# Optimization experiments

Hardware: AMD Instinct MI355X
Metric: run time of the kernel (lower is better)

Reference implementation:

```python
import jax, jax.numpy as jnp
import numpy as np

D_MODEL = 512
D_FF = 2048
VOCAB = 32000
B, N = 2, 384
EPS = 1e-6


def positional_encoding(n, d):
    pos = np.arange(n)[:, None].astype(np.float64)
    i = np.arange(d)[None, :]
    ang = pos / np.power(10000.0, (2 * (i // 2)) / np.float32(d))
    ang[:, 0::2] = np.sin(ang[:, 0::2])
    ang[:, 1::2] = np.cos(ang[:, 1::2])
    return jnp.asarray(ang, dtype=jnp.float32)  # [n, d]


def layer_norm(x, gamma, beta):
    mu = jnp.mean(x, axis=-1, keepdims=True)
    var = jnp.mean(jnp.square(x - mu), axis=-1, keepdims=True)
    return (x - mu) / jnp.sqrt(var + EPS) * gamma + beta


def setup_inputs() -> dict:
    key = jax.random.key(0)
    ks = jax.random.split(key, 12)
    s = 0.02
    return {
        "tokens": jax.random.randint(ks[0], (B, N), 0, VOCAB, dtype=jnp.int32),
        "emb": jax.random.normal(ks[1], (VOCAB, D_MODEL), jnp.float32) * s,
        "Wq": jax.random.normal(ks[2], (D_MODEL, D_MODEL), jnp.float32) * s,
        "bq": jnp.zeros((D_MODEL,), jnp.float32),
        "Wk": jax.random.normal(ks[3], (D_MODEL, D_MODEL), jnp.float32) * s,
        "bk": jnp.zeros((D_MODEL,), jnp.float32),
        "Wv": jax.random.normal(ks[4], (D_MODEL, D_MODEL), jnp.float32) * s,
        "bv": jnp.zeros((D_MODEL,), jnp.float32),
        "attn_scale": jax.random.normal(ks[5], (D_MODEL,), jnp.float32) * 0.05,
        "Wo": jax.random.normal(ks[6], (D_MODEL, D_MODEL), jnp.float32) * s,
        "bo": jnp.zeros((D_MODEL,), jnp.float32),
        "g1": jnp.ones((D_MODEL,), jnp.float32),
        "beta1": jnp.zeros((D_MODEL,), jnp.float32),
        "W1": jax.random.normal(ks[7], (D_MODEL, D_FF), jnp.float32) * s,
        "bf1": jnp.zeros((D_FF,), jnp.float32),
        "W2": jax.random.normal(ks[8], (D_FF, D_MODEL), jnp.float32) * s,
        "bf2": jnp.zeros((D_MODEL,), jnp.float32),
        "g2": jnp.ones((D_MODEL,), jnp.float32),
        "beta2": jnp.zeros((D_MODEL,), jnp.float32),
    }


def reference(tokens, emb, Wq, bq, Wk, bk, Wv, bv, attn_scale, Wo, bo,
              g1, beta1, W1, bf1, W2, bf2, g2, beta2):
    # Embedding + scaled positional encoding
    x = emb[tokens] * jnp.sqrt(jnp.float32(D_MODEL))  # [B, N, D]
    x = x + positional_encoding(N, D_MODEL)[None, :, :]

    # Additive (Bahdanau) self-attention
    q = x @ Wq + bq
    k = x @ Wk + bk  # note: original swaps key/value Dense layers; math-equivalent
    v = x @ Wv + bv
    # scores[b,i,j] = sum_d scale[d] * tanh(q[b,i,d] + k[b,j,d])  -> [B,N,N]
    scores = jnp.einsum("d,bijd->bij", attn_scale,
                        jnp.tanh(q[:, :, None, :] + k[:, None, :, :]))
    weights = jax.nn.softmax(scores, axis=-1)
    attn = jnp.einsum("bij,bjd->bid", weights, v)
    attn = attn @ Wo + bo
    x = layer_norm(x + attn, g1, beta1)

    # Feedforward + residual + LayerNorm
    h = jax.nn.relu(x @ W1 + bf1)
    y = h @ W2 + bf2
    return layer_norm(x + y, g2, beta2)
```

## Files before the change

### kernel.cpp

```cpp
#include <hip/hip_runtime.h>
#include <hip/hip_bf16.h>
#include <math.h>

#define D_MODEL 512
#define D_FF    2048
#define NBATCH  2
#define NSEQ    384
#define NROWS   (NBATCH * NSEQ)
#define LN_EPS  1e-6f

typedef __attribute__((ext_vector_type(8))) short short8;
typedef __attribute__((ext_vector_type(4))) short short4v;
typedef __attribute__((ext_vector_type(4))) float f32x4;
typedef __hip_bfloat16 bf16;

static __device__ __forceinline__ short bfb(float x) {
    bf16 h = __float2bfloat16(x);
    return *reinterpret_cast<short*>(&h);
}

__global__ __launch_bounds__(256) void wt_all_kernel(
    const float* __restrict__ Wq, const float* __restrict__ Wk,
    const float* __restrict__ Wv, const float* __restrict__ Wo,
    const float* __restrict__ W1, const float* __restrict__ W2,
    bf16* __restrict__ wqt, bf16* __restrict__ wkt, bf16* __restrict__ wvt,
    bf16* __restrict__ wot, bf16* __restrict__ w1t, bf16* __restrict__ w2t)
{
    int t = blockIdx.x;
    const float* W; bf16* Wt; int K, N, bx, by;
    if (t < 1024) {
        int w = t >> 8, rem = t & 255;
        W  = (w == 0) ? Wq  : (w == 1) ? Wk  : (w == 2) ? Wv  : Wo;
        Wt = (w == 0) ? wqt : (w == 1) ? wkt : (w == 2) ? wvt : wot;
        K = 512; N = 512; bx = rem & 15; by = rem >> 4;
    } else if (t < 2048) {
        int rem = t - 1024;
        W = W1; Wt = w1t; K = 512; N = 2048; bx = rem & 63; by = rem >> 6;
    } else {
        int rem = t - 2048;
        W = W2; Wt = w2t; K = 2048; N = 512; bx = rem & 15; by = rem >> 4;
    }

    __shared__ float tile[32][33];
    int tx = threadIdx.x & 31, ty = threadIdx.x >> 5;
    #pragma unroll
    for (int r = ty; r < 32; r += 8)
        tile[r][tx] = W[(size_t)(by * 32 + r) * N + bx * 32 + tx];
    __syncthreads();
    #pragma unroll
    for (int r = ty; r < 32; r += 8)
        Wt[(size_t)(bx * 32 + r) * K + by * 32 + tx] = __float2bfloat16(tile[tx][r]);
}

__global__ __launch_bounds__(256) void embed_pe_kernel(
    const int* __restrict__ tokens, const float* __restrict__ emb,
    float* __restrict__ x, bf16* __restrict__ xb)
{
    int row = blockIdx.x;
    int n   = row % NSEQ;
    int tok = tokens[row];
    const float sqrtD = 22.627416997969522f;
    for (int d = threadIdx.x; d < D_MODEL; d += 256) {
        float e = emb[tok * D_MODEL + d] * sqrtD;
        int   i2   = d & ~1;
        float expo = (float)i2 / (float)D_MODEL;
        float ang  = (float)n * powf(10000.0f, -expo);
        float pe   = (d & 1) ? cosf(ang) : sinf(ang);
        float val  = e + pe;
        x [(size_t)row * D_MODEL + d] = val;
        xb[(size_t)row * D_MODEL + d] = __float2bfloat16(val);
    }
}

__global__ __launch_bounds__(256) void qkv_mfma_kernel(
    const bf16* __restrict__ A,
    const bf16* __restrict__ wqt, const bf16* __restrict__ wkt, const bf16* __restrict__ wvt,
    const float* __restrict__ bq, const float* __restrict__ bk, const float* __restrict__ bv,
    float* __restrict__ aexp, float* __restrict__ bexp, bf16* __restrict__ vT)
{
    int z = blockIdx.z;
    const bf16*  Wt   = (z == 0) ? wqt : (z == 1) ? wkt : wvt;
    const float* bias = (z == 0) ? bq  : (z == 1) ? bk  : bv;

    int lane = threadIdx.x & 63, wid = threadIdx.x >> 6;
    int rowBase = blockIdx.y * 32 + (wid >> 1) * 16;
    int colBase = blockIdx.x * 64 + (wid & 1) * 32;

    const bf16* Ap  = A  + (size_t)(rowBase + (lane & 15)) * D_MODEL + ((lane >> 4) << 3);
    const bf16* Bp0 = Wt + (size_t)(colBase + (lane & 15)) * D_MODEL + ((lane >> 4) << 3);
    const bf16* Bp1 = Bp0 + (size_t)16 * D_MODEL;

    f32x4 acc0 = {0.f, 0.f, 0.f, 0.f};
    f32x4 acc1 = {0.f, 0.f, 0.f, 0.f};

    #pragma unroll 4
    for (int k0 = 0; k0 < D_MODEL; k0 += 32) {
        short8 a  = *reinterpret_cast<const short8*>(Ap  + k0);
        short8 b0 = *reinterpret_cast<const short8*>(Bp0 + k0);
        short8 b1 = *reinterpret_cast<const short8*>(Bp1 + k0);
        acc0 = __builtin_amdgcn_mfma_f32_16x16x32_bf16(a, b0, acc0, 0, 0, 0);
        acc1 = __builtin_amdgcn_mfma_f32_16x16x32_bf16(a, b1, acc1, 0, 0, 0);
    }

    int crow = rowBase + ((lane >> 4) << 2);
    int ccol = colBase + (lane & 15);

    if (z < 2) {
        float* C = (z == 0) ? aexp : bexp;
        #pragma unroll
        for (int r = 0; r < 4; ++r) {
            int row = crow + r;
            #pragma unroll
            for (int j = 0; j < 2; ++j) {
                int col = ccol + j * 16;
                float val = (j == 0 ? acc0[r] : acc1[r]) + bias[col];
                C[(size_t)row * D_MODEL + col] = __expf(2.0f * val);
            }
        }
    } else {
        int bb = crow / NSEQ;
        int jr = crow - bb * NSEQ;
        #pragma unroll
        for (int j = 0; j < 2; ++j) {
            int col = ccol + j * 16;
            short4v pk;
            #pragma unroll
            for (int r = 0; r < 4; ++r)
                pk[r] = bfb((j == 0 ? acc0[r] : acc1[r]) + bias[col]);
            size_t idx = ((size_t)bb * D_MODEL + col) * NSEQ + jr;
            *reinterpret_cast<short4v*>((short*)vT + idx) = pk;
        }
    }
}

__global__ __launch_bounds__(512) void score_kernel(
    const float* __restrict__ aexp, const float* __restrict__ bexp,
    const float* __restrict__ scale, bf16* __restrict__ E,
    float* __restrict__ Sp)
{
    int ip   = blockIdx.x;
    int half = blockIdx.y;
    int row0 = ip * 2;
    int b    = row0 / NSEQ;
    int tid  = threadIdx.x;
    int lane = tid & 63, wid = tid >> 6;

    __shared__ float sred[8][2];

    const float* a0p = aexp + (size_t)row0 * D_MODEL + lane * 8;
    float4 A0 = *(const float4*)(a0p);
    float4 A1 = *(const float4*)(a0p + 4);
    float4 B0 = *(const float4*)(a0p + D_MODEL);
    float4 B1 = *(const float4*)(a0p + D_MODEL + 4);
    const float* sp0 = scale + lane * 8;
    float4 S0 = *(const float4*)(sp0);
    float4 S1 = *(const float4*)(sp0 + 4);
    float a0[8] = {A0.x,A0.y,A0.z,A0.w,A1.x,A1.y,A1.z,A1.w};
    float a1[8] = {B0.x,B0.y,B0.z,B0.w,B1.x,B1.y,B1.z,B1.w};
    float sv[8] = {-2.0f*S0.x,-2.0f*S0.y,-2.0f*S0.z,-2.0f*S0.w,
                   -2.0f*S1.x,-2.0f*S1.y,-2.0f*S1.z,-2.0f*S1.w};

    const float* kb = bexp + (size_t)b * NSEQ * D_MODEL + lane * 8;
    int jb = half * 192 + wid;

    float es0 = 0.0f, es1 = 0.0f;

    for (int t = 0; t < 24; t += 2) {
        int j0 = jb + t * 8;
        int j1 = j0 + 8;
        const float4* kp0 = (const float4*)(kb + (size_t)j0 * D_MODEL);
        const float4* kp1 = (const float4*)(kb + (size_t)j1 * D_MODEL);
        float4 x0v = kp0[0], x1v = kp0[1];
        float4 y0v = kp1[0], y1v = kp1[1];
        float b0[8] = {x0v.x,x0v.y,x0v.z,x0v.w,x1v.x,x1v.y,x1v.z,x1v.w};
        float b1[8] = {y0v.x,y0v.y,y0v.z,y0v.w,y1v.x,y1v.y,y1v.z,y1v.w};

        float t00 = 0.f, t01 = 0.f, t10 = 0.f, t11 = 0.f;
        #pragma unroll
        for (int u = 0; u < 8; ++u) {
            float r0 = __builtin_amdgcn_rcpf(fmaf(a0[u], b0[u], 1.0f));
            float r1 = __builtin_amdgcn_rcpf(fmaf(a1[u], b0[u], 1.0f));
            float r2 = __builtin_amdgcn_rcpf(fmaf(a0[u], b1[u], 1.0f));
            float r3 = __builtin_amdgcn_rcpf(fmaf(a1[u], b1[u], 1.0f));
            t00 = fmaf(sv[u], r0, t00);
            t01 = fmaf(sv[u], r1, t01);
            t10 = fmaf(sv[u], r2, t10);
            t11 = fmaf(sv[u], r3, t11);
        }
        #pragma unroll
        for (int off = 1; off < 64; off <<= 1) {
            t00 += __shfl_xor(t00, off, 64);
            t01 += __shfl_xor(t01, off, 64);
            t10 += __shfl_xor(t10, off, 64);
            t11 += __shfl_xor(t11, off, 64);
        }
        float e00 = __expf(t00);
        float e01 = __expf(t01);
        float e10 = __expf(t10);
        float e11 = __expf(t11);
        if (lane == 0) {
            E[(size_t)row0 * NSEQ + j0]       = __float2bfloat16(e00);
            E[(size_t)(row0 + 1) * NSEQ + j0] = __float2bfloat16(e01);
            E[(size_t)row0 * NSEQ + j1]       = __float2bfloat16(e10);
            E[(size_t)(row0 + 1) * NSEQ + j1] = __float2bfloat16(e11);
        }
        es0 += e00 + e10;
        es1 += e01 + e11;
    }

    if (lane == 0) { sred[wid][0] = es0; sred[wid][1] = es1; }
    __syncthreads();
    if (tid < 2) {
        float s = 0.0f;
        #pragma unroll
        for (int w = 0; w < 8; ++w) s += sred[w][tid];
        Sp[(size_t)(row0 + tid) * 2 + half] = s;
    }
}

__global__ __launch_bounds__(256) void pv_mfma_kernel(
    const bf16* __restrict__ E, const bf16* __restrict__ vT,
    const float* __restrict__ Sp, bf16* __restrict__ attnb)
{
    int z = blockIdx.z;
    int lane = threadIdx.x & 63, wid = threadIdx.x >> 6;
    int rowBase = blockIdx.y * 32 + (wid >> 1) * 16;
    int colBase = blockIdx.x * 64 + (wid & 1) * 32;

    const bf16* Ap  = E  + ((size_t)z * NSEQ + rowBase + (lane & 15)) * NSEQ + ((lane >> 4) << 3);
    const bf16* Bp0 = vT + ((size_t)z * D_MODEL + colBase + (lane & 15)) * NSEQ + ((lane >> 4) << 3);
    const bf16* Bp1 = Bp0 + (size_t)16 * NSEQ;

    f32x4 acc0 = {0.f, 0.f, 0.f, 0.f};
    f32x4 acc1 = {0.f, 0.f, 0.f, 0.f};

    #pragma unroll 4
    for (int k0 = 0; k0 < NSEQ; k0 += 32) {
        short8 a  = *reinterpret_cast<const short8*>(Ap  + k0);
        short8 b0 = *reinterpret_cast<const short8*>(Bp0 + k0);
        short8 b1 = *reinterpret_cast<const short8*>(Bp1 + k0);
        acc0 = __builtin_amdgcn_mfma_f32_16x16x32_bf16(a, b0, acc0, 0, 0, 0);
        acc1 = __builtin_amdgcn_mfma_f32_16x16x32_bf16(a, b1, acc1, 0, 0, 0);
    }

    int crow = rowBase + ((lane >> 4) << 2);
    int ccol = colBase + (lane & 15);
    #pragma unroll
    for (int r = 0; r < 4; ++r) {
        int grow = z * NSEQ + crow + r;
        float Sinv = 1.0f / (Sp[(size_t)grow * 2] + Sp[(size_t)grow * 2 + 1]);
        #pragma unroll
        for (int j = 0; j < 2; ++j)
            attnb[(size_t)grow * D_MODEL + ccol + j * 16] =
                __float2bfloat16((j == 0 ? acc0[r] : acc1[r]) * Sinv);
    }
}

__global__ __launch_bounds__(256) void mfma_gemm_kernel(
    const bf16* __restrict__ A, const bf16* __restrict__ Wt,
    const float* __restrict__ bias, const float* __restrict__ resid,
    float* __restrict__ Cf, bf16* __restrict__ Cb,
    int K, int N, int relu)
{
    int lane = threadIdx.x & 63, wid = threadIdx.x >> 6;
    int rowBase = blockIdx.y * 32 + (wid >> 1) * 16;
    int colBase = blockIdx.x * 64 + (wid & 1) * 32;

    const bf16* Ap  = A  + (size_t)(rowBase + (lane & 15)) * K + ((lane >> 4) << 3);
    const bf16* Bp0 = Wt + (size_t)(colBase + (lane & 15)) * K + ((lane >> 4) << 3);
    const bf16* Bp1 = Bp0 + (size_t)16 * K;

    f32x4 acc0 = {0.f, 0.f, 0.f, 0.f};
    f32x4 acc1 = {0.f, 0.f, 0.f, 0.f};

    #pragma unroll 4
    for (int k0 = 0; k0 < K; k0 += 32) {
        short8 a  = *reinterpret_cast<const short8*>(Ap  + k0);
        short8 b0 = *reinterpret_cast<const short8*>(Bp0 + k0);
        short8 b1 = *reinterpret_cast<const short8*>(Bp1 + k0);
        acc0 = __builtin_amdgcn_mfma_f32_16x16x32_bf16(a, b0, acc0, 0, 0, 0);
        acc1 = __builtin_amdgcn_mfma_f32_16x16x32_bf16(a, b1, acc1, 0, 0, 0);
    }

    int crow = rowBase + ((lane >> 4) << 2);
    int ccol = colBase + (lane & 15);
    #pragma unroll
    for (int r = 0; r < 4; ++r) {
        int row = crow + r;
        #pragma unroll
        for (int j = 0; j < 2; ++j) {
            int col = ccol + j * 16;
            float val = (j == 0 ? acc0[r] : acc1[r]) + bias[col];
            if (resid) val += resid[(size_t)row * N + col];
            if (relu)  val = fmaxf(val, 0.0f);
            if (Cf) Cf[(size_t)row * N + col] = val;
            if (Cb) Cb[(size_t)row * N + col] = __float2bfloat16(val);
        }
    }
}

__global__ __launch_bounds__(256) void ln_kernel(
    const float* __restrict__ in, const float* __restrict__ gamma,
    const float* __restrict__ beta, float* __restrict__ out,
    bf16* __restrict__ outb)
{
    int row = blockIdx.x;
    int tid = threadIdx.x;
    int lane = tid & 63, wid = tid >> 6;
    __shared__ float red[4];

    float v0 = in[(size_t)row * D_MODEL + tid];
    float v1 = in[(size_t)row * D_MODEL + tid + 256];

    float s = v0 + v1;
    #pragma unroll
    for (int off = 32; off; off >>= 1) s += __shfl_xor(s, off, 64);
    if (lane == 0) red[wid] = s;
    __syncthreads();
    if (tid == 0) red[0] = red[0] + red[1] + red[2] + red[3];
    __syncthreads();
    float mu = red[0] * (1.0f / D_MODEL);
    __syncthreads();

    float d0 = v0 - mu, d1 = v1 - mu;
    float s2 = d0 * d0 + d1 * d1;
    #pragma unroll
    for (int off = 32; off; off >>= 1) s2 += __shfl_xor(s2, off, 64);
    if (lane == 0) red[wid] = s2;
    __syncthreads();
    if (tid == 0) red[0] = red[0] + red[1] + red[2] + red[3];
    __syncthreads();
    float var = red[0] * (1.0f / D_MODEL);
    float inv = rsqrtf(var + LN_EPS);

    float o0 = d0 * inv * gamma[tid] + beta[tid];
    float o1 = d1 * inv * gamma[tid + 256] + beta[tid + 256];
    out[(size_t)row * D_MODEL + tid]       = o0;
    out[(size_t)row * D_MODEL + tid + 256] = o1;
    if (outb) {
        outb[(size_t)row * D_MODEL + tid]       = __float2bfloat16(o0);
        outb[(size_t)row * D_MODEL + tid + 256] = __float2bfloat16(o1);
    }
}

extern "C" void kernel_launch(void* const* d_in, const int* in_sizes, int n_in,
                              void* d_out, int out_size, void* d_ws, size_t ws_size,
                              hipStream_t stream)
{
    const int*   tokens = (const int*)  d_in[0];
    const float* emb    = (const float*)d_in[1];
    const float* Wq     = (const float*)d_in[2];
    const float* bq     = (const float*)d_in[3];
    const float* Wk     = (const float*)d_in[4];
    const float* bk     = (const float*)d_in[5];
    const float* Wv     = (const float*)d_in[6];
    const float* bv     = (const float*)d_in[7];
    const float* ascale = (const float*)d_in[8];
    const float* Wo     = (const float*)d_in[9];
    const float* bo     = (const float*)d_in[10];
    const float* g1     = (const float*)d_in[11];
    const float* beta1  = (const float*)d_in[12];
    const float* W1     = (const float*)d_in[13];
    const float* bf1    = (const float*)d_in[14];
    const float* W2     = (const float*)d_in[15];
    const float* bf2    = (const float*)d_in[16];
    const float* g2     = (const float*)d_in[17];
    const float* beta2  = (const float*)d_in[18];

    float* out = (float*)d_out;
    float* ws  = (float*)d_ws;

    const size_t SZ = (size_t)NROWS * D_MODEL;

    float* x0   = ws;
    float* aexp = ws + 1 * SZ;
    float* bexp = ws + 2 * SZ;
    float* t1 = aexp;
    float* x1 = bexp;
    float* y  = x0;

    bf16* x0b   = (bf16*)(ws + 3 * SZ);
    bf16* attnb = x0b + SZ;
    bf16* x1b   = attnb + SZ;
    bf16* hb    = x1b + SZ;
    bf16* Eb    = hb + (size_t)NROWS * D_FF;
    bf16* vTb   = Eb + (size_t)NBATCH * NSEQ * NSEQ;
    bf16* wqt   = vTb + (size_t)NBATCH * D_MODEL * NSEQ;
    bf16* wkt   = wqt + (size_t)D_MODEL * D_MODEL;
    bf16* wvt   = wkt + (size_t)D_MODEL * D_MODEL;
    bf16* wot   = wvt + (size_t)D_MODEL * D_MODEL;
    bf16* w1t   = wot + (size_t)D_MODEL * D_MODEL;
    bf16* w2t   = w1t + (size_t)D_MODEL * D_FF;
    float* Sp   = (float*)(w2t + (size_t)D_FF * D_MODEL);

    wt_all_kernel<<<3072, 256, 0, stream>>>(Wq, Wk, Wv, Wo, W1, W2,
                                            wqt, wkt, wvt, wot, w1t, w2t);

    embed_pe_kernel<<<NROWS, 256, 0, stream>>>(tokens, emb, x0, x0b);

    qkv_mfma_kernel<<<dim3(D_MODEL / 64, NROWS / 32, 3), 256, 0, stream>>>(
        x0b, wqt, wkt, wvt, bq, bk, bv, aexp, bexp, vTb);

    score_kernel<<<dim3(NROWS / 2, 2), 512, 0, stream>>>(aexp, bexp, ascale, Eb, Sp);

    pv_mfma_kernel<<<dim3(D_MODEL / 64, NSEQ / 32, NBATCH), 256, 0, stream>>>(
        Eb, vTb, Sp, attnb);

    mfma_gemm_kernel<<<dim3(D_MODEL / 64, NROWS / 32), 256, 0, stream>>>(
        attnb, wot, bo, x0, t1, nullptr, D_MODEL, D_MODEL, 0);

    ln_kernel<<<NROWS, 256, 0, stream>>>(t1, g1, beta1, x1, x1b);

    mfma_gemm_kernel<<<dim3(D_FF / 64, NROWS / 32), 256, 0, stream>>>(
        x1b, w1t, bf1, nullptr, nullptr, hb, D_MODEL, D_FF, 1);

    mfma_gemm_kernel<<<dim3(D_MODEL / 64, NROWS / 32), 256, 0, stream>>>(
        hb, w2t, bf2, x1, y, nullptr, D_FF, D_MODEL, 0);

    ln_kernel<<<NROWS, 256, 0, stream>>>(y, g2, beta2, out, nullptr);
}
```

Before: 129.9 us.

## Pair reciprocals in score kernel, tile 4 query rows, fuse prep kernels

The score kernel now handles 4 query rows per block and splits keys into 4 quarters. It combines two tanh-reciprocal terms into one rcp by computing (s0*q + s1*p)/(p*q), which roughly halves the transcendental reciprocal count and reuses each loaded key row across more queries. The weight transpose and embedding/positional-encoding kernels are merged into one launch, and PE now uses exp2 and fast sin/cos intrinsics. The tradeoffs are extra register pressure from 4 rows of a-values, and possible precision loss or overflow from the product p*q.

```diff
diff --git a/kernel.cpp b/kernel.cpp
--- a/kernel.cpp
+++ b/kernel.cpp
@@ -19,56 +19,54 @@
     return *reinterpret_cast<short*>(&h);
 }
 
-__global__ __launch_bounds__(256) void wt_all_kernel(
+__global__ __launch_bounds__(256) void prep_kernel(
+    const int* __restrict__ tokens, const float* __restrict__ emb,
     const float* __restrict__ Wq, const float* __restrict__ Wk,
     const float* __restrict__ Wv, const float* __restrict__ Wo,
     const float* __restrict__ W1, const float* __restrict__ W2,
     bf16* __restrict__ wqt, bf16* __restrict__ wkt, bf16* __restrict__ wvt,
-    bf16* __restrict__ wot, bf16* __restrict__ w1t, bf16* __restrict__ w2t)
-{
+    bf16* __restrict__ wot, bf16* __restrict__ w1t, bf16* __restrict__ w2t,
+    float* __restrict__ x, bf16* __restrict__ xb)
+{
+    __shared__ float tile[32][33];
     int t = blockIdx.x;
-    const float* W; bf16* Wt; int K, N, bx, by;
-    if (t < 1024) {
-        int w = t >> 8, rem = t & 255;
-        W  = (w == 0) ? Wq  : (w == 1) ? Wk  : (w == 2) ? Wv  : Wo;
-        Wt = (w == 0) ? wqt : (w == 1) ? wkt : (w == 2) ? wvt : wot;
-        K = 512; N = 512; bx = rem & 15; by = rem >> 4;
-    } else if (t < 2048) {
-        int rem = t - 1024;
-        W = W1; Wt = w1t; K = 512; N = 2048; bx = rem & 63; by = rem >> 6;
+
+    if (t < 3072) {
+        const float* W; bf16* Wt; int K, N, bx, by;
+        if (t < 1024) {
+            int w = t >> 8, rem = t & 255;
+            W  = (w == 0) ? Wq  : (w == 1) ? Wk  : (w == 2) ? Wv  : Wo;
+            Wt = (w == 0) ? wqt : (w == 1) ? wkt : (w == 2) ? wvt : wot;
+            K = 512; N = 512; bx = rem & 15; by = rem >> 4;
+        } else if (t < 2048) {
+            int rem = t - 1024;
+            W = W1; Wt = w1t; K = 512; N = 2048; bx = rem & 63; by = rem >> 6;
+        } else {
+            int rem = t - 2048;
+            W = W2; Wt = w2t; K = 2048; N = 512; bx = rem & 15; by = rem >> 4;
+        }
+        int tx = threadIdx.x & 31, ty = threadIdx.x >> 5;
+        #pragma unroll
+        for (int r = ty; r < 32; r += 8)
+            tile[r][tx] = W[(size_t)(by * 32 + r) * N + bx * 32 + tx];
+        __syncthreads();
+        #pragma unroll
+        for (int r = ty; r < 32; r += 8)
+            Wt[(size_t)(bx * 32 + r) * K + by * 32 + tx] = __float2bfloat16(tile[tx][r]);
     } else {
-        int rem = t - 2048;
-        W = W2; Wt = w2t; K = 2048; N = 512; bx = rem & 15; by = rem >> 4;
-    }
-
-    __shared__ float tile[32][33];
-    int tx = threadIdx.x & 31, ty = threadIdx.x >> 5;
-    #pragma unroll
-    for (int r = ty; r < 32; r += 8)
-        tile[r][tx] = W[(size_t)(by * 32 + r) * N + bx * 32 + tx];
-    __syncthreads();
-    #pragma unroll
-    for (int r = ty; r < 32; r += 8)
-        Wt[(size_t)(bx * 32 + r) * K + by * 32 + tx] = __float2bfloat16(tile[tx][r]);
-}
-
-__global__ __launch_bounds__(256) void embed_pe_kernel(
-    const int* __restrict__ tokens, const float* __restrict__ emb,
-    float* __restrict__ x, bf16* __restrict__ xb)
-{
-    int row = blockIdx.x;
-    int n   = row % NSEQ;
-    int tok = tokens[row];
-    const float sqrtD = 22.627416997969522f;
-    for (int d = threadIdx.x; d < D_MODEL; d += 256) {
-        float e = emb[tok * D_MODEL + d] * sqrtD;
-        int   i2   = d & ~1;
-        float expo = (float)i2 / (float)D_MODEL;
-        float ang  = (float)n * powf(10000.0f, -expo);
-        float pe   = (d & 1) ? cosf(ang) : sinf(ang);
-        float val  = e + pe;
-        x [(size_t)row * D_MODEL + d] = val;
-        xb[(size_t)row * D_MODEL + d] = __float2bfloat16(val);
+        int row = t - 3072;
+        int n   = row % NSEQ;
+        int tok = tokens[row];
+        const float sqrtD = 22.627416997969522f;
+        const float ESC   = 0.02595256324130752f;
+        for (int d = threadIdx.x; d < D_MODEL; d += 256) {
+            float e   = emb[tok * D_MODEL + d] * sqrtD;
+            float ang = (float)n * __builtin_amdgcn_exp2f(-(float)(d & ~1) * ESC);
+            float pe  = (d & 1) ? __cosf(ang) : __sinf(ang);
+            float val = e + pe;
+            x [(size_t)row * D_MODEL + d] = val;
+            xb[(size_t)row * D_MODEL + d] = __float2bfloat16(val);
+        }
     }
 }
 
@@ -138,83 +136,93 @@
     const float* __restrict__ scale, bf16* __restrict__ E,
     float* __restrict__ Sp)
 {
-    int ip   = blockIdx.x;
-    int half = blockIdx.y;
-    int row0 = ip * 2;
+    int ig   = blockIdx.x;
+    int qt   = blockIdx.y;
+    int row0 = ig * 4;
     int b    = row0 / NSEQ;
     int tid  = threadIdx.x;
     int lane = tid & 63, wid = tid >> 6;
 
-    __shared__ float sred[8][2];
-
-    const float* a0p = aexp + (size_t)row0 * D_MODEL + lane * 8;
-    float4 A0 = *(const float4*)(a0p);
-    float4 A1 = *(const float4*)(a0p + 4);
-    float4 B0 = *(const float4*)(a0p + D_MODEL);
-    float4 B1 = *(const float4*)(a0p + D_MODEL + 4);
-    const float* sp0 = scale + lane * 8;
-    float4 S0 = *(const float4*)(sp0);
-    float4 S1 = *(const float4*)(sp0 + 4);
-    float a0[8] = {A0.x,A0.y,A0.z,A0.w,A1.x,A1.y,A1.z,A1.w};
-    float a1[8] = {B0.x,B0.y,B0.z,B0.w,B1.x,B1.y,B1.z,B1.w};
+    __shared__ float sred[8][4];
+
+    const float* ap = aexp + (size_t)row0 * D_MODEL + lane * 8;
+    float a[4][8];
+    #pragma unroll
+    for (int r = 0; r < 4; ++r) {
+        float4 A0 = *(const float4*)(ap + (size_t)r * D_MODEL);
+        float4 A1 = *(const float4*)(ap + (size_t)r * D_MODEL + 4);
+        a[r][0]=A0.x; a[r][1]=A0.y; a[r][2]=A0.z; a[r][3]=A0.w;
+        a[r][4]=A1.x; a[r][5]=A1.y; a[r][6]=A1.z; a[r][7]=A1.w;
+    }
+    float4 S0 = *(const float4*)(scale + lane * 8);
+    float4 S1 = *(const float4*)(scale + lane * 8 + 4);
     float sv[8] = {-2.0f*S0.x,-2.0f*S0.y,-2.0f*S0.z,-2.0f*S0.w,
                    -2.0f*S1.x,-2.0f*S1.y,-2.0f*S1.z,-2.0f*S1.w};
 
     const float* kb = bexp + (size_t)b * NSEQ * D_MODEL + lane * 8;
-    int jb = half * 192 + wid;
-
-    float es0 = 0.0f, es1 = 0.0f;
-
-    for (int t = 0; t < 24; t += 2) {
-        int j0 = jb + t * 8;
+    int jb = qt * 96 + wid;
+
+    float es[4] = {0.f, 0.f, 0.f, 0.f};
+
+    for (int t6 = 0; t6 < 6; ++t6) {
+        int j0 = jb + t6 * 16;
         int j1 = j0 + 8;
         const float4* kp0 = (const float4*)(kb + (size_t)j0 * D_MODEL);
         const float4* kp1 = (const float4*)(kb + (size_t)j1 * D_MODEL);
-        float4 x0v = kp0[0], x1v = kp0[1];
-        float4 y0v = kp1[0], y1v = kp1[1];
-        float b0[8] = {x0v.x,x0v.y,x0v.z,x0v.w,x1v.x,x1v.y,x1v.z,x1v.w};
-        float b1[8] = {y0v.x,y0v.y,y0v.z,y0v.w,y1v.x,y1v.y,y1v.z,y1v.w};
-
-        float t00 = 0.f, t01 = 0.f, t10 = 0.f, t11 = 0.f;
-        #pragma unroll
-        for (int u = 0; u < 8; ++u) {
-            float r0 = __builtin_amdgcn_rcpf(fmaf(a0[u], b0[u], 1.0f));
-            float r1 = __builtin_amdgcn_rcpf(fmaf(a1[u], b0[u], 1.0f));
-            float r2 = __builtin_amdgcn_rcpf(fmaf(a0[u], b1[u], 1.0f));
-            float r3 = __builtin_amdgcn_rcpf(fmaf(a1[u], b1[u], 1.0f));
-            t00 = fmaf(sv[u], r0, t00);
-            t01 = fmaf(sv[u], r1, t01);
-            t10 = fmaf(sv[u], r2, t10);
-            t11 = fmaf(sv[u], r3, t11);
-        }
+        float4 xa = kp0[0], xc = kp0[1];
+        float4 ya = kp1[0], yc = kp1[1];
+        float b0[8] = {xa.x,xa.y,xa.z,xa.w,xc.x,xc.y,xc.z,xc.w};
+        float b1[8] = {ya.x,ya.y,ya.z,ya.w,yc.x,yc.y,yc.z,yc.w};
+
+        float u[4][2] = {};
+        #pragma unroll
+        for (int up = 0; up < 4; ++up) {
+            int d0 = up * 2, d1 = d0 + 1;
+            #pragma unroll
+            for (int js = 0; js < 2; ++js) {
+                float xx = js ? b1[d0] : b0[d0];
+                float yy = js ? b1[d1] : b0[d1];
+                #pragma unroll
+                for (int r = 0; r < 4; ++r) {
+                    float p   = fmaf(a[r][d0], xx, 1.0f);
+                    float q   = fmaf(a[r][d1], yy, 1.0f);
+                    float num = fmaf(sv[d0], q, sv[d1] * p);
+                    u[r][js]  = fmaf(num, __builtin_amdgcn_rcpf(p * q), u[r][js]);
+                }
+            }
+        }
+
         #pragma unroll
         for (int off = 1; off < 64; off <<= 1) {
-            t00 += __shfl_xor(t00, off, 64);
-            t01 += __shfl_xor(t01, off, 64);
-            t10 += __shfl_xor(t10, off, 64);
-            t11 += __shfl_xor(t11, off, 64);
-        }
-        float e00 = __expf(t00);
-        float e01 = __expf(t01);
-        float e10 = __expf(t10);
-        float e11 = __expf(t11);
-        if (lane == 0) {
-            E[(size_t)row0 * NSEQ + j0]       = __float2bfloat16(e00);
-            E[(size_t)(row0 + 1) * NSEQ + j0] = __float2bfloat16(e01);
-            E[(size_t)row0 * NSEQ + j1]       = __float2bfloat16(e10);
-            E[(size_t)(row0 + 1) * NSEQ + j1] = __float2bfloat16(e11);
-        }
-        es0 += e00 + e10;
-        es1 += e01 + e11;
-    }
-
-    if (lane == 0) { sred[wid][0] = es0; sred[wid][1] = es1; }
-    __syncthreads();
-    if (tid < 2) {
+            #pragma unroll
+            for (int r = 0; r < 4; ++r) {
+                u[r][0] += __shfl_xor(u[r][0], off, 64);
+                u[r][1] += __shfl_xor(u[r][1], off, 64);
+            }
+        }
+
+        #pragma unroll
+        for (int r = 0; r < 4; ++r) {
+            float e0 = __expf(u[r][0]);
+            float e1 = __expf(u[r][1]);
+            if (lane == 0) {
+                E[(size_t)(row0 + r) * NSEQ + j0] = __float2bfloat16(e0);
+                E[(size_t)(row0 + r) * NSEQ + j1] = __float2bfloat16(e1);
+            }
+            es[r] += e0 + e1;
+        }
+    }
+
+    if (lane == 0) {
+        sred[wid][0] = es[0]; sred[wid][1] = es[1];
+        sred[wid][2] = es[2]; sred[wid][3] = es[3];
+    }
+    __syncthreads();
+    if (tid < 4) {
         float s = 0.0f;
         #pragma unroll
         for (int w = 0; w < 8; ++w) s += sred[w][tid];
-        Sp[(size_t)(row0 + tid) * 2 + half] = s;
+        Sp[(size_t)(row0 + tid) * 4 + qt] = s;
     }
 }
 
@@ -248,7 +256,8 @@
     #pragma unroll
     for (int r = 0; r < 4; ++r) {
         int grow = z * NSEQ + crow + r;
-        float Sinv = 1.0f / (Sp[(size_t)grow * 2] + Sp[(size_t)grow * 2 + 1]);
+        float4 sp4 = *(const float4*)(Sp + (size_t)grow * 4);
+        float Sinv = 1.0f / (sp4.x + sp4.y + sp4.z + sp4.w);
         #pragma unroll
         for (int j = 0; j < 2; ++j)
             attnb[(size_t)grow * D_MODEL + ccol + j * 16] =
@@ -393,15 +402,14 @@
     bf16* w2t   = w1t + (size_t)D_MODEL * D_FF;
     float* Sp   = (float*)(w2t + (size_t)D_FF * D_MODEL);
 
-    wt_all_kernel<<<3072, 256, 0, stream>>>(Wq, Wk, Wv, Wo, W1, W2,
-                                            wqt, wkt, wvt, wot, w1t, w2t);
-
-    embed_pe_kernel<<<NROWS, 256, 0, stream>>>(tokens, emb, x0, x0b);
+    prep_kernel<<<3072 + NROWS, 256, 0, stream>>>(
+        tokens, emb, Wq, Wk, Wv, Wo, W1, W2,
+        wqt, wkt, wvt, wot, w1t, w2t, x0, x0b);
 
     qkv_mfma_kernel<<<dim3(D_MODEL / 64, NROWS / 32, 3), 256, 0, stream>>>(
         x0b, wqt, wkt, wvt, bq, bk, bv, aexp, bexp, vTb);
 
-    score_kernel<<<dim3(NROWS / 2, 2), 512, 0, stream>>>(aexp, bexp, ascale, Eb, Sp);
+    score_kernel<<<dim3(NROWS / 4, 4), 512, 0, stream>>>(aexp, bexp, ascale, Eb, Sp);
 
     pv_mfma_kernel<<<dim3(D_MODEL / 64, NSEQ / 32, NBATCH), 256, 0, stream>>>(
         Eb, vTb, Sp, attnb);
```

Result: faster. 125.8 us (-3.1%).
